# Kernel optimization log

Measured on AMD Instinct MI355X. Metric: run time of the kernel, lower is better.

## Reference

```python
import jax, jax.numpy as jnp
import numpy as np

E, H = 1024, 16
D = E // H


def softmax_1(x):
    # softmax_1: exp(x_i) / (1 + sum_j exp(x_j)), computed stably
    m = jnp.max(x, axis=-1, keepdims=True)
    e = jnp.exp(x - m)
    return e / (jnp.exp(-m) + jnp.sum(e, axis=-1, keepdims=True))


def setup_inputs() -> dict:
    key = jax.random.key(0)
    ks = jax.random.split(key, 8)
    S, B = 1024, 4
    x = jax.random.normal(ks[0], (S, B, E), dtype=jnp.float32)
    attn_bias = jax.random.normal(ks[1], (B, H, S, S), dtype=jnp.float32)
    attn_bias_mul = jax.random.uniform(ks[2], (B, H, S, S), dtype=jnp.float32)
    key_padding_mask = jax.random.randint(ks[3], (B, S), 0, 2).astype(jnp.bool_)
    # xavier-ish init for linear layers (torch Linear: y = x @ W.T + b)
    W_in = jax.random.normal(ks[4], (3 * E, E), dtype=jnp.float32) * (E ** -0.5)
    b_in = jnp.zeros((3 * E,), dtype=jnp.float32)
    W_out = jax.random.normal(ks[5], (E, E), dtype=jnp.float32) * (E ** -0.5)
    b_out = jnp.zeros((E,), dtype=jnp.float32)
    return {"x": x, "attn_bias": attn_bias, "attn_bias_mul": attn_bias_mul,
            "key_padding_mask": key_padding_mask,
            "W_in": W_in, "b_in": b_in, "W_out": W_out, "b_out": b_out}


def reference(x, attn_bias, attn_bias_mul, key_padding_mask, W_in, b_in, W_out, b_out):
    S, B, _ = x.shape
    # in_proj -> [S, B, 3E] -> [B*H, S, 3D]
    qkv = x @ W_in.T + b_in
    qkv = qkv.reshape(S, B * H, 3 * D).transpose(1, 0, 2)
    q, k, v = jnp.split(qkv, 3, axis=-1)
    q = q * (D ** -0.5)
    # scores [B*H, S, S] with additive bias
    aw = jnp.einsum('bqd,bkd->bqk', q, k) + attn_bias.reshape(B * H, S, S)
    # key padding mask (dropout p=0 -> identity)
    kpm = key_padding_mask[:, None, None, :]  # [B,1,1,S]
    aw = jnp.where(kpm, -jnp.inf, aw.reshape(B, H, S, S)).reshape(B * H, S, S)
    abm = jnp.where(kpm, 0.0, attn_bias_mul).reshape(B * H, S, S)
    p = softmax_1(aw) * abm
    attn = jnp.einsum('bqk,bkd->bqd', p, v)  # [B*H, S, D]
    attn = attn.transpose(1, 0, 2).reshape(S, B, E)
    return attn @ W_out.T + b_out
```

## Files before the change

kernel.cpp:

```cpp
#include <hip/hip_runtime.h>
#include <stdint.h>
#include <stddef.h>

typedef __attribute__((ext_vector_type(4))) float f32x4;
typedef __attribute__((ext_vector_type(4))) int   i32x4;
typedef __attribute__((ext_vector_type(8))) short s16x8;
typedef __attribute__((ext_vector_type(4))) short s16x4;
typedef __attribute__((ext_vector_type(8))) __bf16 bf16x8;

#define AS3 __attribute__((address_space(3)))
#define AS1 __attribute__((address_space(1)))

__device__ inline void gload16(const void* g, void* l) {
  __builtin_amdgcn_global_load_lds((AS1 const void*)g, (AS3 void*)l, 16, 0, 0);
}

__device__ inline f32x4 mfma16(s16x8 a, s16x8 b, f32x4 c) {
  return __builtin_amdgcn_mfma_f32_16x16x32_bf16(
      __builtin_bit_cast(bf16x8, a), __builtin_bit_cast(bf16x8, b), c, 0, 0, 0);
}

__device__ inline short f2bf(float f) {
  unsigned u = __builtin_bit_cast(unsigned, f);
  u += 0x7FFFu + ((u >> 16) & 1u);
  return (short)(u >> 16);
}
__device__ inline float bf2f(short x) {
  unsigned u = ((unsigned)(unsigned short)x) << 16;
  return __builtin_bit_cast(float, u);
}

__global__ void cast_bf(const float* __restrict__ in, short* __restrict__ out, int n4) {
  int i = blockIdx.x * 256 + threadIdx.x;
  if (i < n4) {
    f32x4 v = *(const f32x4*)(in + (size_t)i * 4);
    s16x4 o;
#pragma unroll
    for (int r = 0; r < 4; ++r) o[r] = f2bf(v[r]);
    *(s16x4*)(out + (size_t)i * 4) = o;
  }
}

template <int OBF>
__global__ __launch_bounds__(256, 2) void gemm_bt(
    const short* __restrict__ A, const short* __restrict__ B,
    const float* __restrict__ bias, void* __restrict__ Cv,
    int M, int N, int K) {
  const int tid = threadIdx.x, w = tid >> 6, lane = tid & 63;
  const int quad = lane >> 4, l15 = lane & 15;
  const int wm = w >> 1, wn = w & 1;
  const int m0 = blockIdx.y * 128, n0 = blockIdx.x * 128;
  __shared__ short As[128 * 32], Bs[128 * 32];
  f32x4 acc[4][4];
#pragma unroll
  for (int i = 0; i < 4; ++i)
#pragma unroll
    for (int j = 0; j < 4; ++j) acc[i][j] = (f32x4){0.f, 0.f, 0.f, 0.f};
  const int rs = lane >> 2, cs = (lane & 3) * 8;
  const int nkt = K >> 5;
  for (int kt = 0; kt < nkt; ++kt) {
    const int k0 = kt * 32;
#pragma unroll
    for (int j = 0; j < 2; ++j) {
      gload16(A + (size_t)(m0 + w * 32 + j * 16 + rs) * K + k0 + cs, &As[w * 1024 + j * 512]);
      gload16(B + (size_t)(n0 + w * 32 + j * 16 + rs) * K + k0 + cs, &Bs[w * 1024 + j * 512]);
    }
    __syncthreads();
    s16x8 af[4], bfr[4];
#pragma unroll
    for (int i = 0; i < 4; ++i) {
      af[i]  = *(const s16x8*)&As[(wm * 64 + i * 16 + l15) * 32 + quad * 8];
      bfr[i] = *(const s16x8*)&Bs[(wn * 64 + i * 16 + l15) * 32 + quad * 8];
    }
#pragma unroll
    for (int ms = 0; ms < 4; ++ms)
#pragma unroll
      for (int ns = 0; ns < 4; ++ns)
        acc[ms][ns] = mfma16(af[ms], bfr[ns], acc[ms][ns]);
    __syncthreads();
  }
#pragma unroll
  for (int ms = 0; ms < 4; ++ms) {
    const int row0 = m0 + wm * 64 + ms * 16 + quad * 4;
#pragma unroll
    for (int ns = 0; ns < 4; ++ns) {
      const int col = n0 + wn * 64 + ns * 16 + l15;
      const float bv = bias[col];
#pragma unroll
      for (int r = 0; r < 4; ++r) {
        float v = acc[ms][ns][r] + bv;
        if (OBF) ((short*)Cv)[(size_t)(row0 + r) * N + col] = f2bf(v);
        else     ((float*)Cv)[(size_t)(row0 + r) * N + col] = v;
      }
    }
  }
}

__global__ void repack_qk(const short* __restrict__ qkv,
                          short* __restrict__ qh, short* __restrict__ kh) {
  int idx = blockIdx.x * 256 + threadIdx.x;
  int dg = idx & 15;
  int ty = (idx >> 4) & 1;
  int s  = (idx >> 5) & 1023;
  int bh = idx >> 15;
  int b_ = bh >> 4, h_ = bh & 15;
  const short* src = qkv + (size_t)(s * 4 + b_) * 3072 + h_ * 192 + ty * 64 + dg * 4;
  s16x4 v = *(const s16x4*)src;
  if (ty == 0) {
#pragma unroll
    for (int i = 0; i < 4; ++i) v[i] = f2bf(bf2f(v[i]) * 0.125f);
    *(s16x4*)&qh[((size_t)bh << 16) + s * 64 + dg * 4] = v;
  } else {
    *(s16x4*)&kh[((size_t)bh << 16) + s * 64 + dg * 4] = v;
  }
}

__global__ void transpose_v(const short* __restrict__ qkv, short* __restrict__ vT) {
  __shared__ short t[64][80];
  int bh = blockIdx.x, st_ = blockIdx.y;
  int b_ = bh >> 4, h_ = bh & 15;
  int tid = threadIdx.x;
#pragma unroll
  for (int p = 0; p < 2; ++p) {
    int s_l = p * 32 + (tid >> 3), ch = tid & 7;
    const short* src = qkv + (size_t)((st_ * 64 + s_l) * 4 + b_) * 3072 + h_ * 192 + 128 + ch * 8;
    *(s16x8*)&t[s_l][ch * 8] = *(const s16x8*)src;
  }
  __syncthreads();
#pragma unroll
  for (int p = 0; p < 2; ++p) {
    int d_l = p * 32 + (tid >> 3), sc = tid & 7;
    s16x8 vv;
#pragma unroll
    for (int j = 0; j < 8; ++j) vv[j] = t[sc * 8 + j][d_l];
    *(s16x8*)&vT[((size_t)bh << 16) + d_l * 1024 + st_ * 64 + sc * 8] = vv;
  }
}

__global__ __launch_bounds__(256, 2) void attn_fused(
    const short* __restrict__ qh, const short* __restrict__ kh,
    const short* __restrict__ vT, const float* __restrict__ bias,
    const float* __restrict__ abm, const int* __restrict__ kpm,
    short* __restrict__ attnbf) {
  const int tid = threadIdx.x;
  const int w = tid >> 6, lane = tid & 63, quad = lane >> 4, l15 = lane & 15;
  const int bh = blockIdx.x, qb = blockIdx.y;
  const int b_ = bh >> 4, h_ = bh & 15;
  const short* qhd = qh + ((size_t)bh << 16);
  const short* khd = kh + ((size_t)bh << 16);
  const short* vTd = vT + ((size_t)bh << 16);
  const float* biasd = bias + ((size_t)bh << 20);
  const float* abmd  = abm  + ((size_t)bh << 20);
  const int*   kpmd  = kpm + (b_ << 10);
  const int qw = qb * 128 + w * 32;

  __shared__ short kbuf[2][32 * 64];
  __shared__ short vbuf[2][64 * 32];
  __shared__ short wl[4][32 * 40];
  __shared__ float alds[4][32];

  s16x8 qf[2][2];
#pragma unroll
  for (int ns = 0; ns < 2; ++ns)
#pragma unroll
    for (int t = 0; t < 2; ++t)
      qf[ns][t] = *(const s16x8*)&qhd[(size_t)(qw + ns * 16 + l15) * 64 + t * 32 + quad * 8];

  f32x4 o[2][4];
#pragma unroll
  for (int ns = 0; ns < 2; ++ns)
#pragma unroll
    for (int ds = 0; ds < 4; ++ds) o[ns][ds] = (f32x4){0.f, 0.f, 0.f, 0.f};
  float mrun[2] = {-1e30f, -1e30f}, lrun[2] = {0.f, 0.f};

  struct Pack { f32x4 bs[2][2]; f32x4 ab[2][2]; i32x4 kp[2]; };
  Pack P0, P1;

  auto stage = [&](int kt, int pb) {
    gload16(khd + (size_t)kt * 2048 + w * 512 + lane * 8, &kbuf[pb][w * 512]);
    gload16(vTd + (size_t)(w * 16 + (lane >> 2)) * 1024 + kt * 32 + (lane & 3) * 8,
            &vbuf[pb][w * 512]);
  };
  auto loadP = [&](int kt, Pack& P) {
    const int kb = kt * 32;
#pragma unroll
    for (int ns = 0; ns < 2; ++ns) {
      const size_t qrow = (size_t)(qw + ns * 16 + l15) * 1024;
#pragma unroll
      for (int ms = 0; ms < 2; ++ms) {
        P.bs[ns][ms] = *(const f32x4*)&biasd[qrow + kb + ms * 16 + quad * 4];
        P.ab[ns][ms] = *(const f32x4*)&abmd [qrow + kb + ms * 16 + quad * 4];
      }
    }
#pragma unroll
    for (int ms = 0; ms < 2; ++ms)
      P.kp[ms] = *(const i32x4*)&kpmd[kb + ms * 16 + quad * 4];
  };

  auto compute = [&](int pb, Pack& P) {
    const f32x4 z4 = {0.f, 0.f, 0.f, 0.f};
    f32x4 st[2][2];
#pragma unroll
    for (int ms = 0; ms < 2; ++ms) {
      s16x8 a0 = *(const s16x8*)&kbuf[pb][(ms * 16 + l15) * 64 + quad * 8];
      s16x8 a1 = *(const s16x8*)&kbuf[pb][(ms * 16 + l15) * 64 + 32 + quad * 8];
#pragma unroll
      for (int ns = 0; ns < 2; ++ns)
        st[ms][ns] = mfma16(a1, qf[ns][1], mfma16(a0, qf[ns][0], z4));
    }
    float mloc[2] = {-1e30f, -1e30f};
#pragma unroll
    for (int ms = 0; ms < 2; ++ms)
#pragma unroll
      for (int ns = 0; ns < 2; ++ns)
#pragma unroll
        for (int r = 0; r < 4; ++r) {
          float sc = st[ms][ns][r] + P.bs[ns][ms][r];
          sc = (P.kp[ms][r] != 0) ? -1e30f : sc;
          st[ms][ns][r] = sc;
          mloc[ns] = fmaxf(mloc[ns], sc);
        }
    float al[2], lloc[2] = {0.f, 0.f};
#pragma unroll
    for (int ns = 0; ns < 2; ++ns) {
      mloc[ns] = fmaxf(mloc[ns], __shfl_xor(mloc[ns], 16));
      mloc[ns] = fmaxf(mloc[ns], __shfl_xor(mloc[ns], 32));
      float mn = fmaxf(mrun[ns], mloc[ns]);
      al[ns] = __expf(mrun[ns] - mn);
      mrun[ns] = mn;
    }
#pragma unroll
    for (int ms = 0; ms < 2; ++ms)
#pragma unroll
      for (int ns = 0; ns < 2; ++ns)
#pragma unroll
        for (int r = 0; r < 4; ++r) {
          float e = (P.kp[ms][r] != 0) ? 0.f : __expf(st[ms][ns][r] - mrun[ns]);
          st[ms][ns][r] = e;
          lloc[ns] += e;
        }
#pragma unroll
    for (int ns = 0; ns < 2; ++ns) {
      lloc[ns] += __shfl_xor(lloc[ns], 16);
      lloc[ns] += __shfl_xor(lloc[ns], 32);
      lrun[ns] = lrun[ns] * al[ns] + lloc[ns];
      alds[w][ns * 16 + l15] = al[ns];
    }
#pragma unroll
    for (int ms = 0; ms < 2; ++ms)
#pragma unroll
      for (int ns = 0; ns < 2; ++ns) {
        s16x4 pk;
#pragma unroll
        for (int r = 0; r < 4; ++r) pk[r] = f2bf(st[ms][ns][r] * P.ab[ns][ms][r]);
        *(s16x4*)&wl[w][(ns * 16 + l15) * 40 + ms * 16 + quad * 4] = pk;
      }
    f32x4 av[2];
    s16x8 pf[2];
#pragma unroll
    for (int ns = 0; ns < 2; ++ns) {
      av[ns] = *(const f32x4*)&alds[w][ns * 16 + quad * 4];
      pf[ns] = *(const s16x8*)&wl[w][(ns * 16 + l15) * 40 + quad * 8];
    }
#pragma unroll
    for (int ns = 0; ns < 2; ++ns)
#pragma unroll
      for (int ds = 0; ds < 4; ++ds) o[ns][ds] *= av[ns];
#pragma unroll
    for (int ds = 0; ds < 4; ++ds) {
      s16x8 vf = *(const s16x8*)&vbuf[pb][(ds * 16 + l15) * 32 + quad * 8];
#pragma unroll
      for (int ns = 0; ns < 2; ++ns) o[ns][ds] = mfma16(pf[ns], vf, o[ns][ds]);
    }
  };

  stage(0, 0);
  loadP(0, P0);
  __syncthreads();
  for (int kt = 0; kt < 32; kt += 2) {
    stage(kt + 1, 1);
    loadP(kt + 1, P1);
    compute(0, P0);
    __syncthreads();
    if (kt + 2 < 32) { stage(kt + 2, 0); loadP(kt + 2, P0); }
    compute(1, P1);
    __syncthreads();
  }

#pragma unroll
  for (int ns = 0; ns < 2; ++ns) {
    float rd = 1.f / (__expf(-mrun[ns]) + lrun[ns]);
    alds[w][ns * 16 + l15] = rd;
  }
  f32x4 rdv[2];
#pragma unroll
  for (int ns = 0; ns < 2; ++ns) rdv[ns] = *(const f32x4*)&alds[w][ns * 16 + quad * 4];
#pragma unroll
  for (int ns = 0; ns < 2; ++ns)
#pragma unroll
    for (int ds = 0; ds < 4; ++ds) {
      f32x4 ov = o[ns][ds] * rdv[ns];
#pragma unroll
      for (int r = 0; r < 4; ++r) {
        int s = qw + ns * 16 + quad * 4 + r;
        attnbf[(size_t)(s * 4 + b_) * 1024 + h_ * 64 + ds * 16 + l15] = f2bf(ov[r]);
      }
    }
}

extern "C" void kernel_launch(void* const* d_in, const int* in_sizes, int n_in,
                              void* d_out, int out_size, void* d_ws, size_t ws_size,
                              hipStream_t stream) {
  const float* x     = (const float*)d_in[0];
  const float* bias  = (const float*)d_in[1];
  const float* abm   = (const float*)d_in[2];
  const int*   kpm   = (const int*)  d_in[3];
  const float* W_in  = (const float*)d_in[4];
  const float* b_in  = (const float*)d_in[5];
  const float* W_out = (const float*)d_in[6];
  const float* b_out = (const float*)d_in[7];
  float* out = (float*)d_out;

  char* ws = (char*)d_ws;
  short* xbf    = (short*)(ws);
  short* wibf   = (short*)(ws + (8u << 20));
  short* wobf   = (short*)(ws + (14u << 20) + (512u << 10));
  short* qkvbf  = (short*)(ws + (16u << 20) + (768u << 10));
  short* qh     = (short*)(ws + (40u << 20) + (768u << 10));
  short* kh     = (short*)(ws + (48u << 20) + (768u << 10));
  short* vTh    = (short*)(ws + (56u << 20) + (768u << 10));
  short* attnbf = (short*)(ws + (64u << 20) + (768u << 10));

  cast_bf<<<4096, 256, 0, stream>>>(x, xbf, 1048576);
  cast_bf<<<3072, 256, 0, stream>>>(W_in, wibf, 786432);
  cast_bf<<<1024, 256, 0, stream>>>(W_out, wobf, 262144);

  gemm_bt<1><<<dim3(24, 32), 256, 0, stream>>>(xbf, wibf, b_in, (void*)qkvbf, 4096, 3072, 1024);

  repack_qk<<<8192, 256, 0, stream>>>(qkvbf, qh, kh);
  transpose_v<<<dim3(64, 16), 256, 0, stream>>>(qkvbf, vTh);

  attn_fused<<<dim3(64, 8), 256, 0, stream>>>(qh, kh, vTh, bias, abm, kpm, attnbf);

  gemm_bt<0><<<dim3(8, 32), 256, 0, stream>>>(attnbf, wobf, b_out, (void*)out, 4096, 1024, 1024);
}
```

Baseline: 641.8 us.

## Merge cast and repack kernels, shrink attention and out-proj tiles for more blocks

Merges the three cast kernels into one launch and the Q/K repack and V transpose into one kernel, which cuts launch count. The attention kernel now gives each wave 16 query rows instead of 32, doubling the grid to 1024 blocks and raising the occupancy hint to 4 blocks per SM, for better latency hiding on the bandwidth-bound bias and multiplier streams. The output projection GEMM uses 64x64 tiles to get more blocks, at the cost of less operand reuse. In attention, K/V tiles staged in shared memory are now reused across fewer query rows, so shared-memory and K/V traffic per query rise.

```diff
diff --git a/kernel.cpp b/kernel.cpp
--- a/kernel.cpp
+++ b/kernel.cpp
@@ -30,61 +30,70 @@
   return __builtin_bit_cast(float, u);
 }
 
-__global__ void cast_bf(const float* __restrict__ in, short* __restrict__ out, int n4) {
+__global__ void cast_all(const float* __restrict__ x, const float* __restrict__ wi,
+                         const float* __restrict__ wo, short* __restrict__ xb,
+                         short* __restrict__ wib, short* __restrict__ wob) {
   int i = blockIdx.x * 256 + threadIdx.x;
-  if (i < n4) {
-    f32x4 v = *(const f32x4*)(in + (size_t)i * 4);
-    s16x4 o;
-#pragma unroll
-    for (int r = 0; r < 4; ++r) o[r] = f2bf(v[r]);
-    *(s16x4*)(out + (size_t)i * 4) = o;
-  }
-}
-
-template <int OBF>
+  const float* src;
+  short* dst;
+  int off;
+  if (i < 1048576)      { src = x;  dst = xb;  off = i; }
+  else if (i < 1835008) { src = wi; dst = wib; off = i - 1048576; }
+  else                  { src = wo; dst = wob; off = i - 1835008; }
+  f32x4 v = *(const f32x4*)(src + (size_t)off * 4);
+  s16x4 o;
+#pragma unroll
+  for (int r = 0; r < 4; ++r) o[r] = f2bf(v[r]);
+  *(s16x4*)(dst + (size_t)off * 4) = o;
+}
+
+template <int OBF, int FR>
 __global__ __launch_bounds__(256, 2) void gemm_bt(
     const short* __restrict__ A, const short* __restrict__ B,
     const float* __restrict__ bias, void* __restrict__ Cv,
     int M, int N, int K) {
+  const int TILE = FR * 32;
   const int tid = threadIdx.x, w = tid >> 6, lane = tid & 63;
   const int quad = lane >> 4, l15 = lane & 15;
   const int wm = w >> 1, wn = w & 1;
-  const int m0 = blockIdx.y * 128, n0 = blockIdx.x * 128;
-  __shared__ short As[128 * 32], Bs[128 * 32];
-  f32x4 acc[4][4];
-#pragma unroll
-  for (int i = 0; i < 4; ++i)
-#pragma unroll
-    for (int j = 0; j < 4; ++j) acc[i][j] = (f32x4){0.f, 0.f, 0.f, 0.f};
+  const int m0 = blockIdx.y * TILE, n0 = blockIdx.x * TILE;
+  __shared__ short As[TILE * 32], Bs[TILE * 32];
+  f32x4 acc[FR][FR];
+#pragma unroll
+  for (int i = 0; i < FR; ++i)
+#pragma unroll
+    for (int j = 0; j < FR; ++j) acc[i][j] = (f32x4){0.f, 0.f, 0.f, 0.f};
   const int rs = lane >> 2, cs = (lane & 3) * 8;
   const int nkt = K >> 5;
   for (int kt = 0; kt < nkt; ++kt) {
     const int k0 = kt * 32;
 #pragma unroll
-    for (int j = 0; j < 2; ++j) {
-      gload16(A + (size_t)(m0 + w * 32 + j * 16 + rs) * K + k0 + cs, &As[w * 1024 + j * 512]);
-      gload16(B + (size_t)(n0 + w * 32 + j * 16 + rs) * K + k0 + cs, &Bs[w * 1024 + j * 512]);
+    for (int j = 0; j < FR / 2; ++j) {
+      gload16(A + (size_t)(m0 + w * (FR * 8) + j * 16 + rs) * K + k0 + cs,
+              &As[w * (FR * 256) + j * 512]);
+      gload16(B + (size_t)(n0 + w * (FR * 8) + j * 16 + rs) * K + k0 + cs,
+              &Bs[w * (FR * 256) + j * 512]);
     }
     __syncthreads();
-    s16x8 af[4], bfr[4];
-#pragma unroll
-    for (int i = 0; i < 4; ++i) {
-      af[i]  = *(const s16x8*)&As[(wm * 64 + i * 16 + l15) * 32 + quad * 8];
-      bfr[i] = *(const s16x8*)&Bs[(wn * 64 + i * 16 + l15) * 32 + quad * 8];
-    }
-#pragma unroll
-    for (int ms = 0; ms < 4; ++ms)
-#pragma unroll
-      for (int ns = 0; ns < 4; ++ns)
+    s16x8 af[FR], bfr[FR];
+#pragma unroll
+    for (int i = 0; i < FR; ++i) {
+      af[i]  = *(const s16x8*)&As[(wm * (FR * 16) + i * 16 + l15) * 32 + quad * 8];
+      bfr[i] = *(const s16x8*)&Bs[(wn * (FR * 16) + i * 16 + l15) * 32 + quad * 8];
+    }
+#pragma unroll
+    for (int ms = 0; ms < FR; ++ms)
+#pragma unroll
+      for (int ns = 0; ns < FR; ++ns)
         acc[ms][ns] = mfma16(af[ms], bfr[ns], acc[ms][ns]);
     __syncthreads();
   }
 #pragma unroll
-  for (int ms = 0; ms < 4; ++ms) {
-    const int row0 = m0 + wm * 64 + ms * 16 + quad * 4;
-#pragma unroll
-    for (int ns = 0; ns < 4; ++ns) {
-      const int col = n0 + wn * 64 + ns * 16 + l15;
+  for (int ms = 0; ms < FR; ++ms) {
+    const int row0 = m0 + wm * (FR * 16) + ms * 16 + quad * 4;
+#pragma unroll
+    for (int ns = 0; ns < FR; ++ns) {
+      const int col = n0 + wn * (FR * 16) + ns * 16 + l15;
       const float bv = bias[col];
 #pragma unroll
       for (int r = 0; r < 4; ++r) {
@@ -96,48 +105,47 @@
   }
 }
 
-__global__ void repack_qk(const short* __restrict__ qkv,
-                          short* __restrict__ qh, short* __restrict__ kh) {
-  int idx = blockIdx.x * 256 + threadIdx.x;
-  int dg = idx & 15;
-  int ty = (idx >> 4) & 1;
-  int s  = (idx >> 5) & 1023;
-  int bh = idx >> 15;
-  int b_ = bh >> 4, h_ = bh & 15;
-  const short* src = qkv + (size_t)(s * 4 + b_) * 3072 + h_ * 192 + ty * 64 + dg * 4;
-  s16x4 v = *(const s16x4*)src;
-  if (ty == 0) {
-#pragma unroll
-    for (int i = 0; i < 4; ++i) v[i] = f2bf(bf2f(v[i]) * 0.125f);
-    *(s16x4*)&qh[((size_t)bh << 16) + s * 64 + dg * 4] = v;
-  } else {
-    *(s16x4*)&kh[((size_t)bh << 16) + s * 64 + dg * 4] = v;
-  }
-}
-
-__global__ void transpose_v(const short* __restrict__ qkv, short* __restrict__ vT) {
+__global__ void repack_all(const short* __restrict__ qkv, short* __restrict__ qh,
+                           short* __restrict__ kh, short* __restrict__ vT) {
   __shared__ short t[64][80];
-  int bh = blockIdx.x, st_ = blockIdx.y;
-  int b_ = bh >> 4, h_ = bh & 15;
-  int tid = threadIdx.x;
-#pragma unroll
-  for (int p = 0; p < 2; ++p) {
-    int s_l = p * 32 + (tid >> 3), ch = tid & 7;
-    const short* src = qkv + (size_t)((st_ * 64 + s_l) * 4 + b_) * 3072 + h_ * 192 + 128 + ch * 8;
-    *(s16x8*)&t[s_l][ch * 8] = *(const s16x8*)src;
+  const int bh = blockIdx.x, st_ = blockIdx.y;
+  const int b_ = bh >> 4, h_ = bh & 15;
+  const int tid = threadIdx.x;
+#pragma unroll
+  for (int part = 0; part < 4; ++part) {
+    int lin = part * 256 + tid;
+    int dg = lin & 7, ty = (lin >> 3) & 1, s_l = lin >> 4;
+    int s = st_ * 64 + s_l;
+    s16x8 v = *(const s16x8*)(qkv + (size_t)(s * 4 + b_) * 3072 + h_ * 192 + ty * 64 + dg * 8);
+    if (ty == 0) {
+#pragma unroll
+      for (int i = 0; i < 8; ++i) v[i] = f2bf(bf2f(v[i]) * 0.125f);
+      *(s16x8*)&qh[((size_t)bh << 16) + (size_t)s * 64 + dg * 8] = v;
+    } else {
+      *(s16x8*)&kh[((size_t)bh << 16) + (size_t)s * 64 + dg * 8] = v;
+    }
+  }
+#pragma unroll
+  for (int part = 0; part < 2; ++part) {
+    int lin = part * 256 + tid;
+    int ch = lin & 7, s_l = lin >> 3;
+    int s = st_ * 64 + s_l;
+    *(s16x8*)&t[s_l][ch * 8] =
+        *(const s16x8*)(qkv + (size_t)(s * 4 + b_) * 3072 + h_ * 192 + 128 + ch * 8);
   }
   __syncthreads();
 #pragma unroll
-  for (int p = 0; p < 2; ++p) {
-    int d_l = p * 32 + (tid >> 3), sc = tid & 7;
+  for (int part = 0; part < 2; ++part) {
+    int lin = part * 256 + tid;
+    int sc = lin & 7, d_l = lin >> 3;
     s16x8 vv;
 #pragma unroll
     for (int j = 0; j < 8; ++j) vv[j] = t[sc * 8 + j][d_l];
-    *(s16x8*)&vT[((size_t)bh << 16) + d_l * 1024 + st_ * 64 + sc * 8] = vv;
-  }
-}
-
-__global__ __launch_bounds__(256, 2) void attn_fused(
+    *(s16x8*)&vT[((size_t)bh << 16) + (size_t)d_l * 1024 + st_ * 64 + sc * 8] = vv;
+  }
+}
+
+__global__ __launch_bounds__(256, 4) void attn_fused(
     const short* __restrict__ qh, const short* __restrict__ kh,
     const short* __restrict__ vT, const float* __restrict__ bias,
     const float* __restrict__ abm, const int* __restrict__ kpm,
@@ -152,28 +160,24 @@
   const float* biasd = bias + ((size_t)bh << 20);
   const float* abmd  = abm  + ((size_t)bh << 20);
   const int*   kpmd  = kpm + (b_ << 10);
-  const int qw = qb * 128 + w * 32;
+  const int qw = qb * 64 + w * 16;
 
   __shared__ short kbuf[2][32 * 64];
   __shared__ short vbuf[2][64 * 32];
-  __shared__ short wl[4][32 * 40];
-  __shared__ float alds[4][32];
-
-  s16x8 qf[2][2];
-#pragma unroll
-  for (int ns = 0; ns < 2; ++ns)
-#pragma unroll
-    for (int t = 0; t < 2; ++t)
-      qf[ns][t] = *(const s16x8*)&qhd[(size_t)(qw + ns * 16 + l15) * 64 + t * 32 + quad * 8];
-
-  f32x4 o[2][4];
-#pragma unroll
-  for (int ns = 0; ns < 2; ++ns)
-#pragma unroll
-    for (int ds = 0; ds < 4; ++ds) o[ns][ds] = (f32x4){0.f, 0.f, 0.f, 0.f};
-  float mrun[2] = {-1e30f, -1e30f}, lrun[2] = {0.f, 0.f};
-
-  struct Pack { f32x4 bs[2][2]; f32x4 ab[2][2]; i32x4 kp[2]; };
+  __shared__ short wl[4][16 * 40];
+  __shared__ float alds[4][16];
+
+  s16x8 qf[2];
+#pragma unroll
+  for (int t = 0; t < 2; ++t)
+    qf[t] = *(const s16x8*)&qhd[(size_t)(qw + l15) * 64 + t * 32 + quad * 8];
+
+  f32x4 o[4];
+#pragma unroll
+  for (int ds = 0; ds < 4; ++ds) o[ds] = (f32x4){0.f, 0.f, 0.f, 0.f};
+  float mrun = -1e30f, lrun = 0.f;
+
+  struct Pack { f32x4 bs[2]; f32x4 ab[2]; i32x4 kp[2]; };
   Pack P0, P1;
 
   auto stage = [&](int kt, int pb) {
@@ -183,94 +187,67 @@
   };
   auto loadP = [&](int kt, Pack& P) {
     const int kb = kt * 32;
-#pragma unroll
-    for (int ns = 0; ns < 2; ++ns) {
-      const size_t qrow = (size_t)(qw + ns * 16 + l15) * 1024;
-#pragma unroll
-      for (int ms = 0; ms < 2; ++ms) {
-        P.bs[ns][ms] = *(const f32x4*)&biasd[qrow + kb + ms * 16 + quad * 4];
-        P.ab[ns][ms] = *(const f32x4*)&abmd [qrow + kb + ms * 16 + quad * 4];
-      }
-    }
-#pragma unroll
-    for (int ms = 0; ms < 2; ++ms)
+    const size_t qrow = (size_t)(qw + l15) * 1024;
+#pragma unroll
+    for (int ms = 0; ms < 2; ++ms) {
+      P.bs[ms] = *(const f32x4*)&biasd[qrow + kb + ms * 16 + quad * 4];
+      P.ab[ms] = *(const f32x4*)&abmd [qrow + kb + ms * 16 + quad * 4];
       P.kp[ms] = *(const i32x4*)&kpmd[kb + ms * 16 + quad * 4];
+    }
   };
 
   auto compute = [&](int pb, Pack& P) {
     const f32x4 z4 = {0.f, 0.f, 0.f, 0.f};
-    f32x4 st[2][2];
+    f32x4 st[2];
 #pragma unroll
     for (int ms = 0; ms < 2; ++ms) {
       s16x8 a0 = *(const s16x8*)&kbuf[pb][(ms * 16 + l15) * 64 + quad * 8];
       s16x8 a1 = *(const s16x8*)&kbuf[pb][(ms * 16 + l15) * 64 + 32 + quad * 8];
-#pragma unroll
-      for (int ns = 0; ns < 2; ++ns)
-        st[ms][ns] = mfma16(a1, qf[ns][1], mfma16(a0, qf[ns][0], z4));
-    }
-    float mloc[2] = {-1e30f, -1e30f};
+      st[ms] = mfma16(a1, qf[1], mfma16(a0, qf[0], z4));
+    }
+    float mloc = -1e30f;
 #pragma unroll
     for (int ms = 0; ms < 2; ++ms)
 #pragma unroll
-      for (int ns = 0; ns < 2; ++ns)
-#pragma unroll
-        for (int r = 0; r < 4; ++r) {
-          float sc = st[ms][ns][r] + P.bs[ns][ms][r];
-          sc = (P.kp[ms][r] != 0) ? -1e30f : sc;
-          st[ms][ns][r] = sc;
-          mloc[ns] = fmaxf(mloc[ns], sc);
-        }
-    float al[2], lloc[2] = {0.f, 0.f};
-#pragma unroll
-    for (int ns = 0; ns < 2; ++ns) {
-      mloc[ns] = fmaxf(mloc[ns], __shfl_xor(mloc[ns], 16));
-      mloc[ns] = fmaxf(mloc[ns], __shfl_xor(mloc[ns], 32));
-      float mn = fmaxf(mrun[ns], mloc[ns]);
-      al[ns] = __expf(mrun[ns] - mn);
-      mrun[ns] = mn;
-    }
+      for (int r = 0; r < 4; ++r) {
+        float sc = st[ms][r] + P.bs[ms][r];
+        sc = (P.kp[ms][r] != 0) ? -1e30f : sc;
+        st[ms][r] = sc;
+        mloc = fmaxf(mloc, sc);
+      }
+    mloc = fmaxf(mloc, __shfl_xor(mloc, 16));
+    mloc = fmaxf(mloc, __shfl_xor(mloc, 32));
+    float mn = fmaxf(mrun, mloc);
+    float al = __expf(mrun - mn);
+    mrun = mn;
+    float lloc = 0.f;
 #pragma unroll
     for (int ms = 0; ms < 2; ++ms)
 #pragma unroll
-      for (int ns = 0; ns < 2; ++ns)
-#pragma unroll
-        for (int r = 0; r < 4; ++r) {
-          float e = (P.kp[ms][r] != 0) ? 0.f : __expf(st[ms][ns][r] - mrun[ns]);
-          st[ms][ns][r] = e;
-          lloc[ns] += e;
-        }
-#pragma unroll
-    for (int ns = 0; ns < 2; ++ns) {
-      lloc[ns] += __shfl_xor(lloc[ns], 16);
-      lloc[ns] += __shfl_xor(lloc[ns], 32);
-      lrun[ns] = lrun[ns] * al[ns] + lloc[ns];
-      alds[w][ns * 16 + l15] = al[ns];
-    }
-#pragma unroll
-    for (int ms = 0; ms < 2; ++ms)
-#pragma unroll
-      for (int ns = 0; ns < 2; ++ns) {
-        s16x4 pk;
-#pragma unroll
-        for (int r = 0; r < 4; ++r) pk[r] = f2bf(st[ms][ns][r] * P.ab[ns][ms][r]);
-        *(s16x4*)&wl[w][(ns * 16 + l15) * 40 + ms * 16 + quad * 4] = pk;
+      for (int r = 0; r < 4; ++r) {
+        float e = (P.kp[ms][r] != 0) ? 0.f : __expf(st[ms][r] - mrun);
+        st[ms][r] = e;
+        lloc += e;
       }
-    f32x4 av[2];
-    s16x8 pf[2];
-#pragma unroll
-    for (int ns = 0; ns < 2; ++ns) {
-      av[ns] = *(const f32x4*)&alds[w][ns * 16 + quad * 4];
-      pf[ns] = *(const s16x8*)&wl[w][(ns * 16 + l15) * 40 + quad * 8];
-    }
-#pragma unroll
-    for (int ns = 0; ns < 2; ++ns)
-#pragma unroll
-      for (int ds = 0; ds < 4; ++ds) o[ns][ds] *= av[ns];
+    lloc += __shfl_xor(lloc, 16);
+    lloc += __shfl_xor(lloc, 32);
+    lrun = lrun * al + lloc;
+    alds[w][l15] = al;
+#pragma unroll
+    for (int ms = 0; ms < 2; ++ms) {
+      s16x4 pk;
+#pragma unroll
+      for (int r = 0; r < 4; ++r) pk[r] = f2bf(st[ms][r] * P.ab[ms][r]);
+      *(s16x4*)&wl[w][l15 * 40 + ms * 16 + quad * 4] = pk;
+    }
+    f32x4 av = *(const f32x4*)&alds[w][quad * 4];
+    s16x8 pf = *(const s16x8*)&wl[w][l15 * 40 + quad * 8];
+#pragma unroll
+    for (int ds = 0; ds < 4; ++ds) o[ds] *= av;
 #pragma unroll
     for (int ds = 0; ds < 4; ++ds) {
       s16x8 vf = *(const s16x8*)&vbuf[pb][(ds * 16 + l15) * 32 + quad * 8];
-#pragma unroll
-      for (int ns = 0; ns < 2; ++ns) o[ns][ds] = mfma16(pf[ns], vf, o[ns][ds]);
+      o[ds] = mfma16(pf, vf, o[ds]);
     }
   };
 
@@ -287,25 +264,18 @@
     __syncthreads();
   }
 
-#pragma unroll
-  for (int ns = 0; ns < 2; ++ns) {
-    float rd = 1.f / (__expf(-mrun[ns]) + lrun[ns]);
-    alds[w][ns * 16 + l15] = rd;
-  }
-  f32x4 rdv[2];
-#pragma unroll
-  for (int ns = 0; ns < 2; ++ns) rdv[ns] = *(const f32x4*)&alds[w][ns * 16 + quad * 4];
-#pragma unroll
-  for (int ns = 0; ns < 2; ++ns)
-#pragma unroll
-    for (int ds = 0; ds < 4; ++ds) {
-      f32x4 ov = o[ns][ds] * rdv[ns];
-#pragma unroll
-      for (int r = 0; r < 4; ++r) {
-        int s = qw + ns * 16 + quad * 4 + r;
-        attnbf[(size_t)(s * 4 + b_) * 1024 + h_ * 64 + ds * 16 + l15] = f2bf(ov[r]);
-      }
-    }
+  float rd = 1.f / (__expf(-mrun) + lrun);
+  alds[w][l15] = rd;
+  f32x4 rdv = *(const f32x4*)&alds[w][quad * 4];
+#pragma unroll
+  for (int ds = 0; ds < 4; ++ds) {
+    f32x4 ov = o[ds] * rdv;
+#pragma unroll
+    for (int r = 0; r < 4; ++r) {
+      int s = qw + quad * 4 + r;
+      attnbf[(size_t)(s * 4 + b_) * 1024 + h_ * 64 + ds * 16 + l15] = f2bf(ov[r]);
+    }
+  }
 }
 
 extern "C" void kernel_launch(void* const* d_in, const int* in_sizes, int n_in,
@@ -331,16 +301,15 @@
   short* vTh    = (short*)(ws + (56u << 20) + (768u << 10));
   short* attnbf = (short*)(ws + (64u << 20) + (768u << 10));
 
-  cast_bf<<<4096, 256, 0, stream>>>(x, xbf, 1048576);
-  cast_bf<<<3072, 256, 0, stream>>>(W_in, wibf, 786432);
-  cast_bf<<<1024, 256, 0, stream>>>(W_out, wobf, 262144);
-
-  gemm_bt<1><<<dim3(24, 32), 256, 0, stream>>>(xbf, wibf, b_in, (void*)qkvbf, 4096, 3072, 1024);
-
-  repack_qk<<<8192, 256, 0, stream>>>(qkvbf, qh, kh);
-  transpose_v<<<dim3(64, 16), 256, 0, stream>>>(qkvbf, vTh);
-
-  attn_fused<<<dim3(64, 8), 256, 0, stream>>>(qh, kh, vTh, bias, abm, kpm, attnbf);
-
-  gemm_bt<0><<<dim3(8, 32), 256, 0, stream>>>(attnbf, wobf, b_out, (void*)out, 4096, 1024, 1024);
-}
+  cast_all<<<8192, 256, 0, stream>>>(x, W_in, W_out, xbf, wibf, wobf);
+
+  gemm_bt<1, 4><<<dim3(24, 32), 256, 0, stream>>>(xbf, wibf, b_in, (void*)qkvbf,
+                                                  4096, 3072, 1024);
+
+  repack_all<<<dim3(64, 16), 256, 0, stream>>>(qkvbf, qh, kh, vTh);
+
+  attn_fused<<<dim3(64, 16), 256, 0, stream>>>(qh, kh, vTh, bias, abm, kpm, attnbf);
+
+  gemm_bt<0, 2><<<dim3(16, 64), 256, 0, stream>>>(attnbf, wobf, b_out, (void*)out,
+                                                  4096, 1024, 1024);
+}
```

Result: faster. 627.3 us (-2.3%).
